# Kernel tuning notes

Hardware: AMD Instinct MI355X
Metric: run time of the kernel (lower is better)

The kernel has to match this reference:

```python
import jax, jax.numpy as jnp
import numpy as np

N, M, H, EMB, F = 2000, 32, 64, 32, 32   # nodes, neighbors, hidden, emb_dim, node_feat_dim
T, B, HOR = 12, 4, 12                     # seq_len, batch, horizon
K = 2                                     # tcn kernel
L_SAGE = 2
DILS = (1, 2)                             # dilations for the 2 TCN blocks


def _causal_conv(x, w, b, d):
    # x: (BN, C, T), w: (C_out, C_in, K) -- causal via left padding (K-1)*d
    y = jax.lax.conv_general_dilated(
        x, w, window_strides=(1,), padding=[((K - 1) * d, 0)],
        rhs_dilation=(d,), dimension_numbers=('NCH', 'OIH', 'NCH'))
    return y + b[None, :, None]


def setup_inputs() -> dict:
    key = jax.random.key(0)
    ks = jax.random.split(key, 32)
    s = 0.05
    def g(i, shape):
        return jax.random.normal(ks[i], shape, dtype=jnp.float32) * s
    return dict(
        inputs=jax.random.normal(ks[0], (T, B, N), dtype=jnp.float32),
        node_feas=jax.random.normal(ks[1], (N, F), dtype=jnp.float32),
        node_index=jax.random.randint(ks[2], (N, M), 0, N),
        # NodeEmbeddingMLP (fc3/fc4/fc5)
        w_fc3=g(3, (F, H)), b_fc3=jnp.zeros((H,), jnp.float32),
        w_fc4=g(4, (H, H)), b_fc4=jnp.zeros((H,), jnp.float32),
        w_fc5=g(5, (H, EMB)), b_fc5=jnp.zeros((EMB,), jnp.float32),
        # node_hidden_proj
        w_nhp=g(6, (EMB, H)), b_nhp=jnp.zeros((H,), jnp.float32),
        # attention (no bias)
        w_q=g(7, (EMB, H)), w_k=g(8, (EMB, H)),
        # input_proj
        w_in=g(9, (1, H)), b_in=jnp.zeros((H,), jnp.float32),
        # GraphSAGE layers (stacked)
        sage_w_self=g(10, (L_SAGE, H, H)), sage_b_self=jnp.zeros((L_SAGE, H), jnp.float32),
        sage_w_neigh=g(11, (L_SAGE, H, H)), sage_b_neigh=jnp.zeros((L_SAGE, H), jnp.float32),
        # TCN: 2 temporal blocks, each with conv1/conv2 (OIH layout)
        tcn_w1=g(12, (2, H, H, K)), tcn_b1=jnp.zeros((2, H), jnp.float32),
        tcn_w2=g(13, (2, H, H, K)), tcn_b2=jnp.zeros((2, H), jnp.float32),
        # scalar gate + output head
        w_gate=g(14, (H, 1)), b_gate=jnp.zeros((1,), jnp.float32),
        w_out=g(15, (H, HOR)), b_out=jnp.zeros((HOR,), jnp.float32),
    )


def reference(inputs, node_feas, node_index,
              w_fc3, b_fc3, w_fc4, b_fc4, w_fc5, b_fc5,
              w_nhp, b_nhp, w_q, w_k, w_in, b_in,
              sage_w_self, sage_b_self, sage_w_neigh, sage_b_neigh,
              tcn_w1, tcn_b1, tcn_w2, tcn_b2,
              w_gate, b_gate, w_out, b_out):
    # --- node embedding MLP ---
    e = jax.nn.relu(node_feas @ w_fc3 + b_fc3)
    e = jax.nn.relu(e @ w_fc4 + b_fc4)
    e = e @ w_fc5 + b_fc5                                  # (N, EMB)

    # --- attention over sampled neighbors (learned slim adjacency) ---
    q = e @ w_q                                            # (N, H)
    k = e[node_index] @ w_k                                # (N, M, H)
    scores = jnp.einsum('nh,nmh->nm', q, k) / jnp.sqrt(jnp.float32(H))
    w_adj = jax.nn.softmax(scores, axis=1)                 # (N, M) rows sum to 1

    node_hidden = e @ w_nhp + b_nhp                        # (N, H)

    # --- reshape inputs: (T, B, N) -> (B, T, N, 1) ---
    x = jnp.transpose(inputs, (1, 0, 2)).reshape(B, T, N, 1)
    x_proj = x @ w_in + b_in                               # (B, T, N, H)
    fused = x_proj + node_hidden                           # broadcast (N, H)
    h = fused.reshape(B * T, N, H)

    # --- GraphSAGE encoder: gather neighbors, weighted aggregate ---
    for l in range(L_SAGE):
        nb = h[:, node_index]                              # (B*T, N, M, H) irregular gather
        agg = jnp.einsum('nm,bnmh->bnh', w_adj, nb)        # (B*T, N, H)
        h = jax.nn.relu(h @ sage_w_self[l] + sage_b_self[l]
                        + agg @ sage_w_neigh[l] + sage_b_neigh[l])

    mid_output = h.reshape(B, T, N, H)

    # --- TCN over time per node: (B*N, H, T) ---
    ht = jnp.transpose(mid_output, (0, 2, 3, 1)).reshape(B * N, H, T)
    for l in range(2):
        res = ht
        y = jax.nn.relu(_causal_conv(ht, tcn_w1[l], tcn_b1[l], DILS[l]))
        y = jax.nn.relu(_causal_conv(y, tcn_w2[l], tcn_b2[l], DILS[l]))
        ht = jax.nn.relu(y + res)

    h_t = ht[:, :, -1]                                     # (B*N, H) last step temporal
    h_s = mid_output[:, -1].reshape(B * N, H)              # (B*N, H) last step spatial
    gate = jax.nn.sigmoid(h_t @ w_gate + b_gate)           # (B*N, 1) scalar gate
    fused_out = gate * h_t + (1.0 - gate) * h_s

    out = fused_out @ w_out + b_out                        # (B*N, HOR)
    outputs = out.reshape(B, N, HOR).transpose(2, 0, 1).reshape(HOR, B, N)
    return outputs, mid_output, w_adj
```

## Files before the change

### kernel.cpp

```cpp
#include <hip/hip_runtime.h>
#include <math.h>


__global__ __launch_bounds__(256) void k_embed(
    const float* __restrict__ nf, const float* __restrict__ inputs,
    const float* __restrict__ w3, const float* __restrict__ b3,
    const float* __restrict__ w4, const float* __restrict__ b4,
    const float* __restrict__ w5, const float* __restrict__ b5,
    const float* __restrict__ wq, const float* __restrict__ wk,
    const float* __restrict__ wn, const float* __restrict__ bn,
    const float* __restrict__ b_in,
    const float* __restrict__ tw1, const float* __restrict__ tw2,
    const float* __restrict__ sws, const float* __restrict__ swn,
    float4* __restrict__ wt4, float4* __restrict__ wsg,
    float* __restrict__ qo, float* __restrict__ eko, float* __restrict__ nho,
    float* __restrict__ xT)
{
    const int tid = threadIdx.x;
    if (tid < 192) {
        const int id = blockIdx.x * 192 + tid;
        const int t = id / 8000, rem = id % 8000;
        const int b = rem / 2000, n2 = rem % 2000;
        xT[n2 * 48 + b * 12 + t] = inputs[id];
    }
    if (blockIdx.x < 32) {
        const int id = blockIdx.x * 256 + tid;
        const int c = id >> 11, rr = id & 2047;
        const int p = rr >> 6, o = rr & 63;
        const float* src = (c == 0) ? tw1 : (c == 1) ? tw2
                         : (c == 2) ? tw1 + 8192 : tw2 + 8192;
        wt4[id] = *(const float4*)(src + o * 128 + p * 4);
    } else if (blockIdx.x < 48) {
        const int id = (blockIdx.x - 32) * 256 + tid;
        const int l = id >> 11, rr = id & 2047;
        const int k2 = rr >> 6, h = rr & 63;
        const float* S = sws + l * 4096;
        const float* Nn = swn + l * 4096;
        wsg[id] = make_float4(S[(2 * k2) * 64 + h],     Nn[(2 * k2) * 64 + h],
                              S[(2 * k2 + 1) * 64 + h], Nn[(2 * k2 + 1) * 64 + h]);
    }
    const int lane = tid & 63;
    const int n = blockIdx.x * 4 + (tid >> 6);

    float nfv = 0.f;
    if (lane < 32) nfv = nf[n * 32 + lane];

    float e1 = b3[lane];
#pragma unroll
    for (int f = 0; f < 32; ++f)
        e1 = fmaf(__shfl(nfv, f), w3[f * 64 + lane], e1);
    e1 = fmaxf(e1, 0.f);

    float e2 = b4[lane];
#pragma unroll
    for (int f = 0; f < 64; ++f)
        e2 = fmaf(__shfl(e1, f), w4[f * 64 + lane], e2);
    e2 = fmaxf(e2, 0.f);

    const int c = lane & 31;
    float ev = b5[c];
#pragma unroll
    for (int f = 0; f < 64; ++f)
        ev = fmaf(__shfl(e2, f), w5[f * 32 + c], ev);

    float qv = 0.f, ekv = 0.f, nhv = bn[lane] + b_in[lane];
#pragma unroll
    for (int f = 0; f < 32; ++f) {
        float e = __shfl(ev, f);
        qv  = fmaf(e, wq[f * 64 + lane], qv);
        ekv = fmaf(e, wk[f * 64 + lane], ekv);
        nhv = fmaf(e, wn[f * 64 + lane], nhv);
    }
    qo [n * 64 + lane] = qv;
    eko[n * 64 + lane] = ekv;
    nho[n * 64 + lane] = nhv;
}

__global__ __launch_bounds__(256) void k_front(
    const float* __restrict__ q, const float* __restrict__ ek,
    const float* __restrict__ xT, const float* __restrict__ nh2,
    const int* __restrict__ nidx,
    const float* __restrict__ sws, const float* __restrict__ sbs,
    const float* __restrict__ swn, const float* __restrict__ sbn,
    const float* __restrict__ w_in, const float4* __restrict__ wsg,
    float* __restrict__ wadj, float2* __restrict__ xa,
    float* __restrict__ base1, float* __restrict__ vecs)
{
    const int tid = threadIdx.x;
    const int lane = tid & 63, wave = tid >> 6;
    if (blockIdx.x == 500) {
        if (wave == 0) {
            const float wv = w_in[lane];
            float s1 = 0.f, n1 = 0.f;
#pragma unroll
            for (int k = 0; k < 64; ++k) {
                const float wkk = __shfl(wv, k);
                s1 = fmaf(wkk, sws[k * 64 + lane], s1);
                n1 = fmaf(wkk, swn[k * 64 + lane], n1);
            }
            vecs[lane] = s1; vecs[64 + lane] = n1;
        }
        return;
    }
    __shared__ __align__(16) float2 pair[4][64];
    const int n = blockIdx.x * 4 + wave;

    int j = 0;
    if (lane < 32) j = nidx[n * 32 + lane];
    float w;
    {
        const float4* qr = (const float4*)(q + n * 64);
        const float4* er = (const float4*)(ek + j * 64);
        float s = 0.f;
#pragma unroll
        for (int u = 0; u < 16; ++u) {
            const float4 a = qr[u], b = er[u];
            s = fmaf(a.x, b.x, s); s = fmaf(a.y, b.y, s);
            s = fmaf(a.z, b.z, s); s = fmaf(a.w, b.w, s);
        }
        s *= 0.125f;
        float mx = s;
#pragma unroll
        for (int d = 16; d >= 1; d >>= 1) mx = fmaxf(mx, __shfl_xor(mx, d));
        const float ex = expf(s - mx);
        float sum = ex;
#pragma unroll
        for (int d = 16; d >= 1; d >>= 1) sum += __shfl_xor(sum, d);
        w = ex / sum;
        if (lane < 32) wadj[n * 32 + lane] = w;
    }
    float ax = 0.f, anh = 0.f;
    const bool act = lane < 48;
#pragma unroll 8
    for (int m = 0; m < 32; ++m) {
        const int jm = __shfl(j, m);
        const float wm = __shfl(w, m);
        const float xv = act ? xT[jm * 48 + lane] : 0.f;
        ax  = fmaf(wm, xv, ax);
        anh = fmaf(wm, nh2[jm * 64 + lane], anh);
    }
    if (act) xa[n * 48 + lane] = make_float2(xT[n * 48 + lane], ax);
    pair[wave][lane] = make_float2(nh2[n * 64 + lane], anh);
    __syncthreads();

    float acc = sbs[lane] + sbn[lane];
    const float2* pw = pair[wave];
#pragma unroll
    for (int k2 = 0; k2 < 32; ++k2) {
        const float4 wv = wsg[k2 * 64 + lane];
        const float4 sv = *(const float4*)(pw + k2 * 2);
        acc = fmaf(sv.x, wv.x, acc); acc = fmaf(sv.y, wv.y, acc);
        acc = fmaf(sv.z, wv.z, acc); acc = fmaf(sv.w, wv.w, acc);
    }
    base1[n * 64 + lane] = acc;
}

__global__ __launch_bounds__(512, 8) void k_sage2(
    const float* __restrict__ base1, const float2* __restrict__ xa,
    const float* __restrict__ vecs,
    const int* __restrict__ nidx, const float* __restrict__ wadj,
    const float4* __restrict__ wsg2,
    const float* __restrict__ sbs, const float* __restrict__ sbn,
    float* __restrict__ mid)
{
    __shared__ __align__(16) float2 svp[48][64];
    const int tid = threadIdx.x, lane = tid & 63;
    const int wave = __builtin_amdgcn_readfirstlane(tid >> 6);
    const int n = blockIdx.x;
    const int bt0 = wave * 6;

    const float s1 = vecs[lane], n1 = vecs[64 + lane];
    const float bs = base1[n * 64 + lane];

    float agg[6] = {0.f, 0.f, 0.f, 0.f, 0.f, 0.f};
#pragma unroll 8
    for (int m = 0; m < 32; ++m) {
        const int j = nidx[n * 32 + m];
        const float w = wadj[n * 32 + m];
        const float bj = base1[j * 64 + lane];
        const float4* xr = (const float4*)(xa + j * 48 + bt0);
        const float4 p0 = xr[0], p1 = xr[1], p2 = xr[2];
        float t;
        t = fmaf(p0.x, s1, fmaf(p0.y, n1, bj)); agg[0] = fmaf(w, fmaxf(t, 0.f), agg[0]);
        t = fmaf(p0.z, s1, fmaf(p0.w, n1, bj)); agg[1] = fmaf(w, fmaxf(t, 0.f), agg[1]);
        t = fmaf(p1.x, s1, fmaf(p1.y, n1, bj)); agg[2] = fmaf(w, fmaxf(t, 0.f), agg[2]);
        t = fmaf(p1.z, s1, fmaf(p1.w, n1, bj)); agg[3] = fmaf(w, fmaxf(t, 0.f), agg[3]);
        t = fmaf(p2.x, s1, fmaf(p2.y, n1, bj)); agg[4] = fmaf(w, fmaxf(t, 0.f), agg[4]);
        t = fmaf(p2.z, s1, fmaf(p2.w, n1, bj)); agg[5] = fmaf(w, fmaxf(t, 0.f), agg[5]);
    }
    {
        const float4* xs = (const float4*)(xa + n * 48 + bt0);
        const float4 q0 = xs[0], q1 = xs[1], q2 = xs[2];
        svp[bt0 + 0][lane] = make_float2(fmaxf(fmaf(q0.x, s1, fmaf(q0.y, n1, bs)), 0.f), agg[0]);
        svp[bt0 + 1][lane] = make_float2(fmaxf(fmaf(q0.z, s1, fmaf(q0.w, n1, bs)), 0.f), agg[1]);
        svp[bt0 + 2][lane] = make_float2(fmaxf(fmaf(q1.x, s1, fmaf(q1.y, n1, bs)), 0.f), agg[2]);
        svp[bt0 + 3][lane] = make_float2(fmaxf(fmaf(q1.z, s1, fmaf(q1.w, n1, bs)), 0.f), agg[3]);
        svp[bt0 + 4][lane] = make_float2(fmaxf(fmaf(q2.x, s1, fmaf(q2.y, n1, bs)), 0.f), agg[4]);
        svp[bt0 + 5][lane] = make_float2(fmaxf(fmaf(q2.z, s1, fmaf(q2.w, n1, bs)), 0.f), agg[5]);
    }
    const float b2 = sbs[64 + lane] + sbn[64 + lane];
    float acc[6] = {b2, b2, b2, b2, b2, b2};
    const float4* wp = wsg2 + lane;
    const float2* s0 = svp[bt0];
#pragma unroll
    for (int k2 = 0; k2 < 32; ++k2) {
        const float4 w4 = wp[k2 * 64];
        const float4 v0 = *(const float4*)(s0 + 0 * 64 + k2 * 2);
        const float4 v1 = *(const float4*)(s0 + 1 * 64 + k2 * 2);
        const float4 v2 = *(const float4*)(s0 + 2 * 64 + k2 * 2);
        const float4 v3 = *(const float4*)(s0 + 3 * 64 + k2 * 2);
        const float4 v4 = *(const float4*)(s0 + 4 * 64 + k2 * 2);
        const float4 v5 = *(const float4*)(s0 + 5 * 64 + k2 * 2);
        acc[0] = fmaf(v0.x, w4.x, fmaf(v0.y, w4.y, fmaf(v0.z, w4.z, fmaf(v0.w, w4.w, acc[0]))));
        acc[1] = fmaf(v1.x, w4.x, fmaf(v1.y, w4.y, fmaf(v1.z, w4.z, fmaf(v1.w, w4.w, acc[1]))));
        acc[2] = fmaf(v2.x, w4.x, fmaf(v2.y, w4.y, fmaf(v2.z, w4.z, fmaf(v2.w, w4.w, acc[2]))));
        acc[3] = fmaf(v3.x, w4.x, fmaf(v3.y, w4.y, fmaf(v3.z, w4.z, fmaf(v3.w, w4.w, acc[3]))));
        acc[4] = fmaf(v4.x, w4.x, fmaf(v4.y, w4.y, fmaf(v4.z, w4.z, fmaf(v4.w, w4.w, acc[4]))));
        acc[5] = fmaf(v5.x, w4.x, fmaf(v5.y, w4.y, fmaf(v5.z, w4.z, fmaf(v5.w, w4.w, acc[5]))));
    }
#pragma unroll
    for (int r = 0; r < 6; ++r)
        mid[((bt0 + r) * 2000 + n) * 64 + lane] = fmaxf(acc[r], 0.f);
}

__global__ __launch_bounds__(256, 8) void k_tcn(
    const float* __restrict__ mid, const float4* __restrict__ wt4,
    const float* __restrict__ tb1, const float* __restrict__ tb2,
    const float* __restrict__ wgate, const float* __restrict__ bgate,
    const float* __restrict__ wout, const float* __restrict__ bout,
    float* __restrict__ outp)
{
    __shared__ __align__(16) float buf[4][7][68];
    const int tid = threadIdx.x, lane = tid & 63;
    const int wv = __builtin_amdgcn_readfirstlane(tid >> 6);
    const int seq = blockIdx.x * 4 + wv;
    const int b = seq / 2000, n = seq - b * 2000;
    const float* __restrict__ xb = mid + ((long)(b * 12) * 2000 + n) * 64;

    const float r0 = xb[ 7 * 128000 + lane];
    const float r1 = xb[ 9 * 128000 + lane];
    const float r2 = xb[11 * 128000 + lane];

    const float bs1 = tb1[lane];
    float y1[6] = {bs1, bs1, bs1, bs1, bs1, bs1};
    const float* __restrict__ xs = xb + 5 * 128000;
#pragma unroll 4
    for (int ig = 0; ig < 16; ++ig) {
        const float4 wA = wt4[(ig * 2 + 0) * 64 + lane];
        const float4 wB = wt4[(ig * 2 + 1) * 64 + lane];
        float4 xu[7];
#pragma unroll
        for (int u = 0; u < 7; ++u)
            xu[u] = *(const float4*)(xs + u * 128000 + ig * 4);
#pragma unroll
        for (int j = 0; j < 6; ++j) {
            float acc = y1[j];
            acc = fmaf(wA.x, xu[j].x, acc); acc = fmaf(wA.y, xu[j + 1].x, acc);
            acc = fmaf(wA.z, xu[j].y, acc); acc = fmaf(wA.w, xu[j + 1].y, acc);
            acc = fmaf(wB.x, xu[j].z, acc); acc = fmaf(wB.y, xu[j + 1].z, acc);
            acc = fmaf(wB.z, xu[j].w, acc); acc = fmaf(wB.w, xu[j + 1].w, acc);
            y1[j] = acc;
        }
    }
#pragma unroll
    for (int j = 0; j < 6; ++j)
        buf[wv][j][lane] = fmaxf(y1[j], 0.f);

    const float bs2 = tb2[lane];
    float a0 = bs2, a1 = bs2, a2 = bs2;
#pragma unroll 4
    for (int ig = 0; ig < 16; ++ig) {
        const float4 wA = wt4[2048 + (ig * 2 + 0) * 64 + lane];
        const float4 wB = wt4[2048 + (ig * 2 + 1) * 64 + lane];
        float4 yv[6];
#pragma unroll
        for (int j = 0; j < 6; ++j)
            yv[j] = *(const float4*)&buf[wv][j][ig * 4];
        a0 = fmaf(wA.x, yv[0].x, a0); a0 = fmaf(wA.y, yv[1].x, a0);
        a0 = fmaf(wA.z, yv[0].y, a0); a0 = fmaf(wA.w, yv[1].y, a0);
        a0 = fmaf(wB.x, yv[0].z, a0); a0 = fmaf(wB.y, yv[1].z, a0);
        a0 = fmaf(wB.z, yv[0].w, a0); a0 = fmaf(wB.w, yv[1].w, a0);
        a1 = fmaf(wA.x, yv[2].x, a1); a1 = fmaf(wA.y, yv[3].x, a1);
        a1 = fmaf(wA.z, yv[2].y, a1); a1 = fmaf(wA.w, yv[3].y, a1);
        a1 = fmaf(wB.x, yv[2].z, a1); a1 = fmaf(wB.y, yv[3].z, a1);
        a1 = fmaf(wB.z, yv[2].w, a1); a1 = fmaf(wB.w, yv[3].w, a1);
        a2 = fmaf(wA.x, yv[4].x, a2); a2 = fmaf(wA.y, yv[5].x, a2);
        a2 = fmaf(wA.z, yv[4].y, a2); a2 = fmaf(wA.w, yv[5].y, a2);
        a2 = fmaf(wB.x, yv[4].z, a2); a2 = fmaf(wB.y, yv[5].z, a2);
        a2 = fmaf(wB.z, yv[4].w, a2); a2 = fmaf(wB.w, yv[5].w, a2);
    }
    const float x20 = fmaxf(fmaxf(a0, 0.f) + r0, 0.f);
    const float x21 = fmaxf(fmaxf(a1, 0.f) + r1, 0.f);
    const float x22 = fmaxf(fmaxf(a2, 0.f) + r2, 0.f);
    buf[wv][0][lane] = x20;
    buf[wv][1][lane] = x21;
    buf[wv][2][lane] = x22;

    const float bs3 = tb1[64 + lane];
    float d0 = bs3, d1 = bs3;
#pragma unroll 4
    for (int ig = 0; ig < 16; ++ig) {
        const float4 wA = wt4[4096 + (ig * 2 + 0) * 64 + lane];
        const float4 wB = wt4[4096 + (ig * 2 + 1) * 64 + lane];
        const float4 x0 = *(const float4*)&buf[wv][0][ig * 4];
        const float4 x1 = *(const float4*)&buf[wv][1][ig * 4];
        const float4 x2 = *(const float4*)&buf[wv][2][ig * 4];
        d0 = fmaf(wA.x, x0.x, d0); d0 = fmaf(wA.y, x1.x, d0);
        d0 = fmaf(wA.z, x0.y, d0); d0 = fmaf(wA.w, x1.y, d0);
        d0 = fmaf(wB.x, x0.z, d0); d0 = fmaf(wB.y, x1.z, d0);
        d0 = fmaf(wB.z, x0.w, d0); d0 = fmaf(wB.w, x1.w, d0);
        d1 = fmaf(wA.x, x1.x, d1); d1 = fmaf(wA.y, x2.x, d1);
        d1 = fmaf(wA.z, x1.y, d1); d1 = fmaf(wA.w, x2.y, d1);
        d1 = fmaf(wB.x, x1.z, d1); d1 = fmaf(wB.y, x2.z, d1);
        d1 = fmaf(wB.z, x1.w, d1); d1 = fmaf(wB.w, x2.w, d1);
    }
    buf[wv][4][lane] = fmaxf(d0, 0.f);
    buf[wv][5][lane] = fmaxf(d1, 0.f);

    const float bs4 = tb2[64 + lane];
    float f = bs4;
#pragma unroll 4
    for (int ig = 0; ig < 16; ++ig) {
        const float4 wA = wt4[6144 + (ig * 2 + 0) * 64 + lane];
        const float4 wB = wt4[6144 + (ig * 2 + 1) * 64 + lane];
        const float4 g0 = *(const float4*)&buf[wv][4][ig * 4];
        const float4 g1 = *(const float4*)&buf[wv][5][ig * 4];
        f = fmaf(wA.x, g0.x, f); f = fmaf(wA.y, g1.x, f);
        f = fmaf(wA.z, g0.y, f); f = fmaf(wA.w, g1.y, f);
        f = fmaf(wB.x, g0.z, f); f = fmaf(wB.y, g1.z, f);
        f = fmaf(wB.z, g0.w, f); f = fmaf(wB.w, g1.w, f);
    }

    const float ht = fmaxf(fmaxf(f, 0.f) + x22, 0.f);
    float p = ht * wgate[lane];
#pragma unroll
    for (int dd = 1; dd < 64; dd <<= 1) p += __shfl_xor(p, dd);
    const float g = 1.f / (1.f + expf(-(p + bgate[0])));
    buf[wv][6][lane] = g * ht + (1.f - g) * r2;
    if (lane < 12) {
        float acc = bout[lane];
#pragma unroll 4
        for (int ig = 0; ig < 16; ++ig) {
            const float4 f4 = *(const float4*)&buf[wv][6][ig * 4];
            acc = fmaf(f4.x, wout[(ig * 4 + 0) * 12 + lane], acc);
            acc = fmaf(f4.y, wout[(ig * 4 + 1) * 12 + lane], acc);
            acc = fmaf(f4.z, wout[(ig * 4 + 2) * 12 + lane], acc);
            acc = fmaf(f4.w, wout[(ig * 4 + 3) * 12 + lane], acc);
        }
        outp[lane * 8000 + seq] = acc;
    }
}

extern "C" void kernel_launch(void* const* d_in, const int* in_sizes, int n_in,
                              void* d_out, int out_size, void* d_ws, size_t ws_size,
                              hipStream_t stream) {
    const float* inputs     = (const float*)d_in[0];
    const float* node_feas  = (const float*)d_in[1];
    const int*   node_index = (const int*)  d_in[2];
    const float* w_fc3 = (const float*)d_in[3];
    const float* b_fc3 = (const float*)d_in[4];
    const float* w_fc4 = (const float*)d_in[5];
    const float* b_fc4 = (const float*)d_in[6];
    const float* w_fc5 = (const float*)d_in[7];
    const float* b_fc5 = (const float*)d_in[8];
    const float* w_nhp = (const float*)d_in[9];
    const float* b_nhp = (const float*)d_in[10];
    const float* w_q   = (const float*)d_in[11];
    const float* w_k   = (const float*)d_in[12];
    const float* w_in  = (const float*)d_in[13];
    const float* b_in  = (const float*)d_in[14];
    const float* sws   = (const float*)d_in[15];
    const float* sbs   = (const float*)d_in[16];
    const float* swn   = (const float*)d_in[17];
    const float* sbn   = (const float*)d_in[18];
    const float* tw1   = (const float*)d_in[19];
    const float* tb1   = (const float*)d_in[20];
    const float* tw2   = (const float*)d_in[21];
    const float* tb2   = (const float*)d_in[22];
    const float* wgate = (const float*)d_in[23];
    const float* bgate = (const float*)d_in[24];
    const float* wout  = (const float*)d_in[25];
    const float* bout  = (const float*)d_in[26];

    float* out  = (float*)d_out;
    float* mid  = out + 96000;
    float* wadj = mid + 6144000;

    float*  q     = (float*)d_ws;
    float*  ek    = q     + 128000;
    float*  nh2   = ek    + 128000;
    float*  base1 = nh2   + 128000;
    float*  xT    = base1 + 128000;
    float2* xa    = (float2*)(xT + 96000);
    float*  vecs  = xT + 96000 + 192000;
    float4* wt4   = (float4*)(vecs + 128);
    float4* wsg   = (float4*)(vecs + 128 + 32768);

    k_embed<<<500, 256, 0, stream>>>(node_feas, inputs, w_fc3, b_fc3, w_fc4, b_fc4,
                                     w_fc5, b_fc5, w_q, w_k, w_nhp, b_nhp, b_in,
                                     tw1, tw2, sws, swn, wt4, wsg,
                                     q, ek, nh2, xT);
    k_front<<<501, 256, 0, stream>>>(q, ek, xT, nh2, node_index,
                                     sws, sbs, swn, sbn, w_in, wsg,
                                     wadj, xa, base1, vecs);
    k_sage2<<<2000, 512, 0, stream>>>(base1, xa, vecs, node_index, wadj,
                                      wsg + 2048, sbs, sbn, mid);
    k_tcn<<<2000, 256, 0, stream>>>(mid, wt4, tb1, tb2,
                                    wgate, bgate, wout, bout, out);
}
```

Baseline: 125.1 us.

## Fuse TCN stage into SAGE layer-2 kernel using shared-memory node tile

Merges the separate TCN kernel into k_sage2. Each block keeps its node's 48 time-batch rows of mid in shared memory, and two waves then run the four causal convolutions, the gate and the output head from LDS instead of rereading mid from global memory. The TCN weights are repacked into a float2 layout so each lane computes two output channels for one batch, and the head reduction becomes a cross-lane shuffle over 12 outputs. This removes a kernel launch and the global reread of mid. The cost is that six of the eight waves idle during the TCN phase, and the larger shared-memory footprint may lower occupancy.

After: 137.7 us. 1.1x slower.

```diff
diff --git a/kernel.cpp b/kernel.cpp
--- a/kernel.cpp
+++ b/kernel.cpp
@@ -12,7 +12,7 @@
     const float* __restrict__ b_in,
     const float* __restrict__ tw1, const float* __restrict__ tw2,
     const float* __restrict__ sws, const float* __restrict__ swn,
-    float4* __restrict__ wt4, float4* __restrict__ wsg,
+    float2* __restrict__ W2, float4* __restrict__ wsg,
     float* __restrict__ qo, float* __restrict__ eko, float* __restrict__ nho,
     float* __restrict__ xT)
 {
@@ -23,15 +23,16 @@
         const int b = rem / 2000, n2 = rem % 2000;
         xT[n2 * 48 + b * 12 + t] = inputs[id];
     }
-    if (blockIdx.x < 32) {
+    if (blockIdx.x < 64) {
         const int id = blockIdx.x * 256 + tid;
-        const int c = id >> 11, rr = id & 2047;
-        const int p = rr >> 6, o = rr & 63;
+        const int c = id >> 12, r = id & 4095;
+        const int ig = r >> 8, o = (r >> 2) & 63, ii = r & 3;
         const float* src = (c == 0) ? tw1 : (c == 1) ? tw2
                          : (c == 2) ? tw1 + 8192 : tw2 + 8192;
-        wt4[id] = *(const float4*)(src + o * 128 + p * 4);
-    } else if (blockIdx.x < 48) {
-        const int id = (blockIdx.x - 32) * 256 + tid;
+        const int i = ig * 4 + ii;
+        W2[id] = make_float2(src[o * 128 + i * 2], src[o * 128 + i * 2 + 1]);
+    } else if (blockIdx.x < 80) {
+        const int id = (blockIdx.x - 64) * 256 + tid;
         const int l = id >> 11, rr = id & 2047;
         const int k2 = rr >> 6, h = rr & 63;
         const float* S = sws + l * 4096;
@@ -155,199 +156,249 @@
     base1[n * 64 + lane] = acc;
 }
 
+__device__ __forceinline__ float conv8(float acc, const float4 wA, const float4 wB,
+                                       const float4 xl, const float4 xr)
+{
+    acc = fmaf(wA.x, xl.x, acc); acc = fmaf(wA.y, xr.x, acc);
+    acc = fmaf(wA.z, xl.y, acc); acc = fmaf(wA.w, xr.y, acc);
+    acc = fmaf(wB.x, xl.z, acc); acc = fmaf(wB.y, xr.z, acc);
+    acc = fmaf(wB.z, xl.w, acc); acc = fmaf(wB.w, xr.w, acc);
+    return acc;
+}
+
 __global__ __launch_bounds__(512, 8) void k_sage2(
     const float* __restrict__ base1, const float2* __restrict__ xa,
     const float* __restrict__ vecs,
     const int* __restrict__ nidx, const float* __restrict__ wadj,
     const float4* __restrict__ wsg2,
     const float* __restrict__ sbs, const float* __restrict__ sbn,
-    float* __restrict__ mid)
-{
-    __shared__ __align__(16) float2 svp[48][64];
-    const int tid = threadIdx.x, lane = tid & 63;
-    const int wave = __builtin_amdgcn_readfirstlane(tid >> 6);
-    const int n = blockIdx.x;
-    const int bt0 = wave * 6;
-
-    const float s1 = vecs[lane], n1 = vecs[64 + lane];
-    const float bs = base1[n * 64 + lane];
-
-    float agg[6] = {0.f, 0.f, 0.f, 0.f, 0.f, 0.f};
-#pragma unroll 8
-    for (int m = 0; m < 32; ++m) {
-        const int j = nidx[n * 32 + m];
-        const float w = wadj[n * 32 + m];
-        const float bj = base1[j * 64 + lane];
-        const float4* xr = (const float4*)(xa + j * 48 + bt0);
-        const float4 p0 = xr[0], p1 = xr[1], p2 = xr[2];
-        float t;
-        t = fmaf(p0.x, s1, fmaf(p0.y, n1, bj)); agg[0] = fmaf(w, fmaxf(t, 0.f), agg[0]);
-        t = fmaf(p0.z, s1, fmaf(p0.w, n1, bj)); agg[1] = fmaf(w, fmaxf(t, 0.f), agg[1]);
-        t = fmaf(p1.x, s1, fmaf(p1.y, n1, bj)); agg[2] = fmaf(w, fmaxf(t, 0.f), agg[2]);
-        t = fmaf(p1.z, s1, fmaf(p1.w, n1, bj)); agg[3] = fmaf(w, fmaxf(t, 0.f), agg[3]);
-        t = fmaf(p2.x, s1, fmaf(p2.y, n1, bj)); agg[4] = fmaf(w, fmaxf(t, 0.f), agg[4]);
-        t = fmaf(p2.z, s1, fmaf(p2.w, n1, bj)); agg[5] = fmaf(w, fmaxf(t, 0.f), agg[5]);
-    }
-    {
-        const float4* xs = (const float4*)(xa + n * 48 + bt0);
-        const float4 q0 = xs[0], q1 = xs[1], q2 = xs[2];
-        svp[bt0 + 0][lane] = make_float2(fmaxf(fmaf(q0.x, s1, fmaf(q0.y, n1, bs)), 0.f), agg[0]);
-        svp[bt0 + 1][lane] = make_float2(fmaxf(fmaf(q0.z, s1, fmaf(q0.w, n1, bs)), 0.f), agg[1]);
-        svp[bt0 + 2][lane] = make_float2(fmaxf(fmaf(q1.x, s1, fmaf(q1.y, n1, bs)), 0.f), agg[2]);
-        svp[bt0 + 3][lane] = make_float2(fmaxf(fmaf(q1.z, s1, fmaf(q1.w, n1, bs)), 0.f), agg[3]);
-        svp[bt0 + 4][lane] = make_float2(fmaxf(fmaf(q2.x, s1, fmaf(q2.y, n1, bs)), 0.f), agg[4]);
-        svp[bt0 + 5][lane] = make_float2(fmaxf(fmaf(q2.z, s1, fmaf(q2.w, n1, bs)), 0.f), agg[5]);
-    }
-    const float b2 = sbs[64 + lane] + sbn[64 + lane];
-    float acc[6] = {b2, b2, b2, b2, b2, b2};
-    const float4* wp = wsg2 + lane;
-    const float2* s0 = svp[bt0];
-#pragma unroll
-    for (int k2 = 0; k2 < 32; ++k2) {
-        const float4 w4 = wp[k2 * 64];
-        const float4 v0 = *(const float4*)(s0 + 0 * 64 + k2 * 2);
-        const float4 v1 = *(const float4*)(s0 + 1 * 64 + k2 * 2);
-        const float4 v2 = *(const float4*)(s0 + 2 * 64 + k2 * 2);
-        const float4 v3 = *(const float4*)(s0 + 3 * 64 + k2 * 2);
-        const float4 v4 = *(const float4*)(s0 + 4 * 64 + k2 * 2);
-        const float4 v5 = *(const float4*)(s0 + 5 * 64 + k2 * 2);
-        acc[0] = fmaf(v0.x, w4.x, fmaf(v0.y, w4.y, fmaf(v0.z, w4.z, fmaf(v0.w, w4.w, acc[0]))));
-        acc[1] = fmaf(v1.x, w4.x, fmaf(v1.y, w4.y, fmaf(v1.z, w4.z, fmaf(v1.w, w4.w, acc[1]))));
-        acc[2] = fmaf(v2.x, w4.x, fmaf(v2.y, w4.y, fmaf(v2.z, w4.z, fmaf(v2.w, w4.w, acc[2]))));
-        acc[3] = fmaf(v3.x, w4.x, fmaf(v3.y, w4.y, fmaf(v3.z, w4.z, fmaf(v3.w, w4.w, acc[3]))));
-        acc[4] = fmaf(v4.x, w4.x, fmaf(v4.y, w4.y, fmaf(v4.z, w4.z, fmaf(v4.w, w4.w, acc[4]))));
-        acc[5] = fmaf(v5.x, w4.x, fmaf(v5.y, w4.y, fmaf(v5.z, w4.z, fmaf(v5.w, w4.w, acc[5]))));
-    }
-#pragma unroll
-    for (int r = 0; r < 6; ++r)
-        mid[((bt0 + r) * 2000 + n) * 64 + lane] = fmaxf(acc[r], 0.f);
-}
-
-__global__ __launch_bounds__(256, 8) void k_tcn(
-    const float* __restrict__ mid, const float4* __restrict__ wt4,
+    const float2* __restrict__ W2,
     const float* __restrict__ tb1, const float* __restrict__ tb2,
     const float* __restrict__ wgate, const float* __restrict__ bgate,
     const float* __restrict__ wout, const float* __restrict__ bout,
-    float* __restrict__ outp)
+    float* __restrict__ mid, float* __restrict__ outp)
 {
-    __shared__ __align__(16) float buf[4][7][68];
+    __shared__ __align__(16) float pool[6144 + 3264];
+    float2* svp  = (float2*)pool;
+    float*  xls2 = pool + 6144;
+    float*  scr  = pool;
+
     const int tid = threadIdx.x, lane = tid & 63;
-    const int wv = __builtin_amdgcn_readfirstlane(tid >> 6);
-    const int seq = blockIdx.x * 4 + wv;
-    const int b = seq / 2000, n = seq - b * 2000;
-    const float* __restrict__ xb = mid + ((long)(b * 12) * 2000 + n) * 64;
-
-    const float r0 = xb[ 7 * 128000 + lane];
-    const float r1 = xb[ 9 * 128000 + lane];
-    const float r2 = xb[11 * 128000 + lane];
-
-    const float bs1 = tb1[lane];
-    float y1[6] = {bs1, bs1, bs1, bs1, bs1, bs1};
-    const float* __restrict__ xs = xb + 5 * 128000;
+    const int wfl = __builtin_amdgcn_readfirstlane(tid >> 6);
+    const int n = blockIdx.x;
+    const int bt0 = wfl * 6;
+
+    {
+        const float s1 = vecs[lane], n1 = vecs[64 + lane];
+        const float bs = base1[n * 64 + lane];
+
+        float agg[6] = {0.f, 0.f, 0.f, 0.f, 0.f, 0.f};
+#pragma unroll 8
+        for (int m = 0; m < 32; ++m) {
+            const int j = nidx[n * 32 + m];
+            const float w = wadj[n * 32 + m];
+            const float bj = base1[j * 64 + lane];
+            const float4* xr = (const float4*)(xa + j * 48 + bt0);
+            const float4 p0 = xr[0], p1 = xr[1], p2 = xr[2];
+            float t;
+            t = fmaf(p0.x, s1, fmaf(p0.y, n1, bj)); agg[0] = fmaf(w, fmaxf(t, 0.f), agg[0]);
+            t = fmaf(p0.z, s1, fmaf(p0.w, n1, bj)); agg[1] = fmaf(w, fmaxf(t, 0.f), agg[1]);
+            t = fmaf(p1.x, s1, fmaf(p1.y, n1, bj)); agg[2] = fmaf(w, fmaxf(t, 0.f), agg[2]);
+            t = fmaf(p1.z, s1, fmaf(p1.w, n1, bj)); agg[3] = fmaf(w, fmaxf(t, 0.f), agg[3]);
+            t = fmaf(p2.x, s1, fmaf(p2.y, n1, bj)); agg[4] = fmaf(w, fmaxf(t, 0.f), agg[4]);
+            t = fmaf(p2.z, s1, fmaf(p2.w, n1, bj)); agg[5] = fmaf(w, fmaxf(t, 0.f), agg[5]);
+        }
+        {
+            const float4* xs = (const float4*)(xa + n * 48 + bt0);
+            const float4 q0 = xs[0], q1 = xs[1], q2 = xs[2];
+            svp[(bt0 + 0) * 64 + lane] = make_float2(fmaxf(fmaf(q0.x, s1, fmaf(q0.y, n1, bs)), 0.f), agg[0]);
+            svp[(bt0 + 1) * 64 + lane] = make_float2(fmaxf(fmaf(q0.z, s1, fmaf(q0.w, n1, bs)), 0.f), agg[1]);
+            svp[(bt0 + 2) * 64 + lane] = make_float2(fmaxf(fmaf(q1.x, s1, fmaf(q1.y, n1, bs)), 0.f), agg[2]);
+            svp[(bt0 + 3) * 64 + lane] = make_float2(fmaxf(fmaf(q1.z, s1, fmaf(q1.w, n1, bs)), 0.f), agg[3]);
+            svp[(bt0 + 4) * 64 + lane] = make_float2(fmaxf(fmaf(q2.x, s1, fmaf(q2.y, n1, bs)), 0.f), agg[4]);
+            svp[(bt0 + 5) * 64 + lane] = make_float2(fmaxf(fmaf(q2.z, s1, fmaf(q2.w, n1, bs)), 0.f), agg[5]);
+        }
+        const float b2 = sbs[64 + lane] + sbn[64 + lane];
+        float acc[6] = {b2, b2, b2, b2, b2, b2};
+        const float4* wp = wsg2 + lane;
+        const float2* s0 = svp + bt0 * 64;
+#pragma unroll
+        for (int k2 = 0; k2 < 32; ++k2) {
+            const float4 w4 = wp[k2 * 64];
+            const float4 v0 = *(const float4*)(s0 + 0 * 64 + k2 * 2);
+            const float4 v1 = *(const float4*)(s0 + 1 * 64 + k2 * 2);
+            const float4 v2 = *(const float4*)(s0 + 2 * 64 + k2 * 2);
+            const float4 v3 = *(const float4*)(s0 + 3 * 64 + k2 * 2);
+            const float4 v4 = *(const float4*)(s0 + 4 * 64 + k2 * 2);
+            const float4 v5 = *(const float4*)(s0 + 5 * 64 + k2 * 2);
+            acc[0] = fmaf(v0.x, w4.x, fmaf(v0.y, w4.y, fmaf(v0.z, w4.z, fmaf(v0.w, w4.w, acc[0]))));
+            acc[1] = fmaf(v1.x, w4.x, fmaf(v1.y, w4.y, fmaf(v1.z, w4.z, fmaf(v1.w, w4.w, acc[1]))));
+            acc[2] = fmaf(v2.x, w4.x, fmaf(v2.y, w4.y, fmaf(v2.z, w4.z, fmaf(v2.w, w4.w, acc[2]))));
+            acc[3] = fmaf(v3.x, w4.x, fmaf(v3.y, w4.y, fmaf(v3.z, w4.z, fmaf(v3.w, w4.w, acc[3]))));
+            acc[4] = fmaf(v4.x, w4.x, fmaf(v4.y, w4.y, fmaf(v4.z, w4.z, fmaf(v4.w, w4.w, acc[4]))));
+            acc[5] = fmaf(v5.x, w4.x, fmaf(v5.y, w4.y, fmaf(v5.z, w4.z, fmaf(v5.w, w4.w, acc[5]))));
+        }
+#pragma unroll
+        for (int r = 0; r < 6; ++r) {
+            const float mv = fmaxf(acc[r], 0.f);
+            mid[((bt0 + r) * 2000 + n) * 64 + lane] = mv;
+            xls2[(bt0 + r) * 68 + lane] = mv;
+        }
+    }
+    __syncthreads();
+    if (wfl >= 2) return;
+
+    const int h = lane >> 1;
+    const int sl = lane & 1;
+    const int b = wfl * 2 + sl;
+    const int obase = h * 2;
+    const float* __restrict__ xrow = xls2 + b * 12 * 68;
+    const float4* __restrict__ Wf4 = (const float4*)W2;
+
+    float y[2][6];
+    {
+        const float2 bv = *(const float2*)(tb1 + obase);
+#pragma unroll
+        for (int j = 0; j < 6; ++j) { y[0][j] = bv.x; y[1][j] = bv.y; }
+    }
 #pragma unroll 4
     for (int ig = 0; ig < 16; ++ig) {
-        const float4 wA = wt4[(ig * 2 + 0) * 64 + lane];
-        const float4 wB = wt4[(ig * 2 + 1) * 64 + lane];
-        float4 xu[7];
-#pragma unroll
-        for (int u = 0; u < 7; ++u)
-            xu[u] = *(const float4*)(xs + u * 128000 + ig * 4);
-#pragma unroll
-        for (int j = 0; j < 6; ++j) {
-            float acc = y1[j];
-            acc = fmaf(wA.x, xu[j].x, acc); acc = fmaf(wA.y, xu[j + 1].x, acc);
-            acc = fmaf(wA.z, xu[j].y, acc); acc = fmaf(wA.w, xu[j + 1].y, acc);
-            acc = fmaf(wB.x, xu[j].z, acc); acc = fmaf(wB.y, xu[j + 1].z, acc);
-            acc = fmaf(wB.z, xu[j].w, acc); acc = fmaf(wB.w, xu[j + 1].w, acc);
-            y1[j] = acc;
-        }
-    }
-#pragma unroll
-    for (int j = 0; j < 6; ++j)
-        buf[wv][j][lane] = fmaxf(y1[j], 0.f);
-
-    const float bs2 = tb2[lane];
-    float a0 = bs2, a1 = bs2, a2 = bs2;
+        const float4 wA0 = Wf4[(ig * 64 + obase + 0) * 2 + 0];
+        const float4 wB0 = Wf4[(ig * 64 + obase + 0) * 2 + 1];
+        const float4 wA1 = Wf4[(ig * 64 + obase + 1) * 2 + 0];
+        const float4 wB1 = Wf4[(ig * 64 + obase + 1) * 2 + 1];
+        {
+            const float4 x5 = *(const float4*)(xrow +  5 * 68 + ig * 4);
+            const float4 x6 = *(const float4*)(xrow +  6 * 68 + ig * 4);
+            const float4 x7 = *(const float4*)(xrow +  7 * 68 + ig * 4);
+            const float4 x8 = *(const float4*)(xrow +  8 * 68 + ig * 4);
+            y[0][0] = conv8(y[0][0], wA0, wB0, x5, x6); y[1][0] = conv8(y[1][0], wA1, wB1, x5, x6);
+            y[0][1] = conv8(y[0][1], wA0, wB0, x6, x7); y[1][1] = conv8(y[1][1], wA1, wB1, x6, x7);
+            y[0][2] = conv8(y[0][2], wA0, wB0, x7, x8); y[1][2] = conv8(y[1][2], wA1, wB1, x7, x8);
+        }
+        {
+            const float4 x8 = *(const float4*)(xrow +  8 * 68 + ig * 4);
+            const float4 x9 = *(const float4*)(xrow +  9 * 68 + ig * 4);
+            const float4 xa2 = *(const float4*)(xrow + 10 * 68 + ig * 4);
+            const float4 xb2 = *(const float4*)(xrow + 11 * 68 + ig * 4);
+            y[0][3] = conv8(y[0][3], wA0, wB0, x8, x9);  y[1][3] = conv8(y[1][3], wA1, wB1, x8, x9);
+            y[0][4] = conv8(y[0][4], wA0, wB0, x9, xa2); y[1][4] = conv8(y[1][4], wA1, wB1, x9, xa2);
+            y[0][5] = conv8(y[0][5], wA0, wB0, xa2, xb2); y[1][5] = conv8(y[1][5], wA1, wB1, xa2, xb2);
+        }
+    }
+#pragma unroll
+    for (int j = 0; j < 6; ++j) {
+        float2 o2;
+        o2.x = fmaxf(y[0][j], 0.f); o2.y = fmaxf(y[1][j], 0.f);
+        *(float2*)&scr[(j * 4 + b) * 68 + obase] = o2;
+    }
+
+    float a2[2][3];
+    {
+        const float2 bv = *(const float2*)(tb2 + obase);
+#pragma unroll
+        for (int v = 0; v < 3; ++v) { a2[0][v] = bv.x; a2[1][v] = bv.y; }
+    }
 #pragma unroll 4
     for (int ig = 0; ig < 16; ++ig) {
-        const float4 wA = wt4[2048 + (ig * 2 + 0) * 64 + lane];
-        const float4 wB = wt4[2048 + (ig * 2 + 1) * 64 + lane];
-        float4 yv[6];
-#pragma unroll
-        for (int j = 0; j < 6; ++j)
-            yv[j] = *(const float4*)&buf[wv][j][ig * 4];
-        a0 = fmaf(wA.x, yv[0].x, a0); a0 = fmaf(wA.y, yv[1].x, a0);
-        a0 = fmaf(wA.z, yv[0].y, a0); a0 = fmaf(wA.w, yv[1].y, a0);
-        a0 = fmaf(wB.x, yv[0].z, a0); a0 = fmaf(wB.y, yv[1].z, a0);
-        a0 = fmaf(wB.z, yv[0].w, a0); a0 = fmaf(wB.w, yv[1].w, a0);
-        a1 = fmaf(wA.x, yv[2].x, a1); a1 = fmaf(wA.y, yv[3].x, a1);
-        a1 = fmaf(wA.z, yv[2].y, a1); a1 = fmaf(wA.w, yv[3].y, a1);
-        a1 = fmaf(wB.x, yv[2].z, a1); a1 = fmaf(wB.y, yv[3].z, a1);
-        a1 = fmaf(wB.z, yv[2].w, a1); a1 = fmaf(wB.w, yv[3].w, a1);
-        a2 = fmaf(wA.x, yv[4].x, a2); a2 = fmaf(wA.y, yv[5].x, a2);
-        a2 = fmaf(wA.z, yv[4].y, a2); a2 = fmaf(wA.w, yv[5].y, a2);
-        a2 = fmaf(wB.x, yv[4].z, a2); a2 = fmaf(wB.y, yv[5].z, a2);
-        a2 = fmaf(wB.z, yv[4].w, a2); a2 = fmaf(wB.w, yv[5].w, a2);
-    }
-    const float x20 = fmaxf(fmaxf(a0, 0.f) + r0, 0.f);
-    const float x21 = fmaxf(fmaxf(a1, 0.f) + r1, 0.f);
-    const float x22 = fmaxf(fmaxf(a2, 0.f) + r2, 0.f);
-    buf[wv][0][lane] = x20;
-    buf[wv][1][lane] = x21;
-    buf[wv][2][lane] = x22;
-
-    const float bs3 = tb1[64 + lane];
-    float d0 = bs3, d1 = bs3;
+        const float4 wA0 = Wf4[((16 + ig) * 64 + obase + 0) * 2 + 0];
+        const float4 wB0 = Wf4[((16 + ig) * 64 + obase + 0) * 2 + 1];
+        const float4 wA1 = Wf4[((16 + ig) * 64 + obase + 1) * 2 + 0];
+        const float4 wB1 = Wf4[((16 + ig) * 64 + obase + 1) * 2 + 1];
+#pragma unroll
+        for (int v = 0; v < 3; ++v) {
+            const float4 pl = *(const float4*)&scr[((2 * v) * 4 + b) * 68 + ig * 4];
+            const float4 pr = *(const float4*)&scr[((2 * v + 1) * 4 + b) * 68 + ig * 4];
+            a2[0][v] = conv8(a2[0][v], wA0, wB0, pl, pr);
+            a2[1][v] = conv8(a2[1][v], wA1, wB1, pl, pr);
+        }
+    }
+    float x22_0, x22_1;
+    {
+        const int TT[3] = {7, 9, 11};
+#pragma unroll
+        for (int v = 0; v < 3; ++v) {
+            const float2 xr2 = *(const float2*)(xrow + TT[v] * 68 + obase);
+            float2 o2;
+            o2.x = fmaxf(fmaxf(a2[0][v], 0.f) + xr2.x, 0.f);
+            o2.y = fmaxf(fmaxf(a2[1][v], 0.f) + xr2.y, 0.f);
+            *(float2*)&scr[((6 + v) * 4 + b) * 68 + obase] = o2;
+            if (v == 2) { x22_0 = o2.x; x22_1 = o2.y; }
+        }
+    }
+
+    float d3[2][2];
+    {
+        const float2 bv = *(const float2*)(tb1 + 64 + obase);
+        d3[0][0] = bv.x; d3[0][1] = bv.x; d3[1][0] = bv.y; d3[1][1] = bv.y;
+    }
 #pragma unroll 4
     for (int ig = 0; ig < 16; ++ig) {
-        const float4 wA = wt4[4096 + (ig * 2 + 0) * 64 + lane];
-        const float4 wB = wt4[4096 + (ig * 2 + 1) * 64 + lane];
-        const float4 x0 = *(const float4*)&buf[wv][0][ig * 4];
-        const float4 x1 = *(const float4*)&buf[wv][1][ig * 4];
-        const float4 x2 = *(const float4*)&buf[wv][2][ig * 4];
-        d0 = fmaf(wA.x, x0.x, d0); d0 = fmaf(wA.y, x1.x, d0);
-        d0 = fmaf(wA.z, x0.y, d0); d0 = fmaf(wA.w, x1.y, d0);
-        d0 = fmaf(wB.x, x0.z, d0); d0 = fmaf(wB.y, x1.z, d0);
-        d0 = fmaf(wB.z, x0.w, d0); d0 = fmaf(wB.w, x1.w, d0);
-        d1 = fmaf(wA.x, x1.x, d1); d1 = fmaf(wA.y, x2.x, d1);
-        d1 = fmaf(wA.z, x1.y, d1); d1 = fmaf(wA.w, x2.y, d1);
-        d1 = fmaf(wB.x, x1.z, d1); d1 = fmaf(wB.y, x2.z, d1);
-        d1 = fmaf(wB.z, x1.w, d1); d1 = fmaf(wB.w, x2.w, d1);
-    }
-    buf[wv][4][lane] = fmaxf(d0, 0.f);
-    buf[wv][5][lane] = fmaxf(d1, 0.f);
-
-    const float bs4 = tb2[64 + lane];
-    float f = bs4;
+        const float4 wA0 = Wf4[((32 + ig) * 64 + obase + 0) * 2 + 0];
+        const float4 wB0 = Wf4[((32 + ig) * 64 + obase + 0) * 2 + 1];
+        const float4 wA1 = Wf4[((32 + ig) * 64 + obase + 1) * 2 + 0];
+        const float4 wB1 = Wf4[((32 + ig) * 64 + obase + 1) * 2 + 1];
+        const float4 p0 = *(const float4*)&scr[(6 * 4 + b) * 68 + ig * 4];
+        const float4 p1 = *(const float4*)&scr[(7 * 4 + b) * 68 + ig * 4];
+        const float4 p2 = *(const float4*)&scr[(8 * 4 + b) * 68 + ig * 4];
+        d3[0][0] = conv8(d3[0][0], wA0, wB0, p0, p1);
+        d3[1][0] = conv8(d3[1][0], wA1, wB1, p0, p1);
+        d3[0][1] = conv8(d3[0][1], wA0, wB0, p1, p2);
+        d3[1][1] = conv8(d3[1][1], wA1, wB1, p1, p2);
+    }
+    {
+        float2 o2;
+        o2.x = fmaxf(d3[0][0], 0.f); o2.y = fmaxf(d3[1][0], 0.f);
+        *(float2*)&scr[(9 * 4 + b) * 68 + obase] = o2;
+        o2.x = fmaxf(d3[0][1], 0.f); o2.y = fmaxf(d3[1][1], 0.f);
+        *(float2*)&scr[(10 * 4 + b) * 68 + obase] = o2;
+    }
+
+    float f0, f1;
+    {
+        const float2 bv = *(const float2*)(tb2 + 64 + obase);
+        f0 = bv.x; f1 = bv.y;
+    }
 #pragma unroll 4
     for (int ig = 0; ig < 16; ++ig) {
-        const float4 wA = wt4[6144 + (ig * 2 + 0) * 64 + lane];
-        const float4 wB = wt4[6144 + (ig * 2 + 1) * 64 + lane];
-        const float4 g0 = *(const float4*)&buf[wv][4][ig * 4];
-        const float4 g1 = *(const float4*)&buf[wv][5][ig * 4];
-        f = fmaf(wA.x, g0.x, f); f = fmaf(wA.y, g1.x, f);
-        f = fmaf(wA.z, g0.y, f); f = fmaf(wA.w, g1.y, f);
-        f = fmaf(wB.x, g0.z, f); f = fmaf(wB.y, g1.z, f);
-        f = fmaf(wB.z, g0.w, f); f = fmaf(wB.w, g1.w, f);
-    }
-
-    const float ht = fmaxf(fmaxf(f, 0.f) + x22, 0.f);
-    float p = ht * wgate[lane];
-#pragma unroll
-    for (int dd = 1; dd < 64; dd <<= 1) p += __shfl_xor(p, dd);
+        const float4 wA0 = Wf4[((48 + ig) * 64 + obase + 0) * 2 + 0];
+        const float4 wB0 = Wf4[((48 + ig) * 64 + obase + 0) * 2 + 1];
+        const float4 wA1 = Wf4[((48 + ig) * 64 + obase + 1) * 2 + 0];
+        const float4 wB1 = Wf4[((48 + ig) * 64 + obase + 1) * 2 + 1];
+        const float4 g0 = *(const float4*)&scr[(9 * 4 + b) * 68 + ig * 4];
+        const float4 g1 = *(const float4*)&scr[(10 * 4 + b) * 68 + ig * 4];
+        f0 = conv8(f0, wA0, wB0, g0, g1);
+        f1 = conv8(f1, wA1, wB1, g0, g1);
+    }
+    const float ht0 = fmaxf(fmaxf(f0, 0.f) + x22_0, 0.f);
+    const float ht1 = fmaxf(fmaxf(f1, 0.f) + x22_1, 0.f);
+
+    const float2 wg2 = *(const float2*)(wgate + obase);
+    float p = ht0 * wg2.x + ht1 * wg2.y;
+#pragma unroll
+    for (int d = 2; d < 64; d <<= 1) p += __shfl_xor(p, d);
     const float g = 1.f / (1.f + expf(-(p + bgate[0])));
-    buf[wv][6][lane] = g * ht + (1.f - g) * r2;
-    if (lane < 12) {
-        float acc = bout[lane];
-#pragma unroll 4
-        for (int ig = 0; ig < 16; ++ig) {
-            const float4 f4 = *(const float4*)&buf[wv][6][ig * 4];
-            acc = fmaf(f4.x, wout[(ig * 4 + 0) * 12 + lane], acc);
-            acc = fmaf(f4.y, wout[(ig * 4 + 1) * 12 + lane], acc);
-            acc = fmaf(f4.z, wout[(ig * 4 + 2) * 12 + lane], acc);
-            acc = fmaf(f4.w, wout[(ig * 4 + 3) * 12 + lane], acc);
-        }
-        outp[lane * 8000 + seq] = acc;
+    const float2 hs = *(const float2*)(xrow + 11 * 68 + obase);
+    const float fo0 = g * ht0 + (1.f - g) * hs.x;
+    const float fo1 = g * ht1 + (1.f - g) * hs.y;
+
+    float po[12];
+    {
+        const float* wr0 = wout + (obase + 0) * 12;
+        const float* wr1 = wout + (obase + 1) * 12;
+#pragma unroll
+        for (int h2 = 0; h2 < 12; ++h2)
+            po[h2] = fo0 * wr0[h2] + fo1 * wr1[h2];
+    }
+#pragma unroll
+    for (int d = 2; d < 64; d <<= 1) {
+#pragma unroll
+        for (int h2 = 0; h2 < 12; ++h2) po[h2] += __shfl_xor(po[h2], d);
+    }
+    if (h == 0) {
+#pragma unroll
+        for (int h2 = 0; h2 < 12; ++h2)
+            outp[h2 * 8000 + b * 2000 + n] = po[h2] + bout[h2];
     }
 }
 
@@ -393,18 +444,18 @@
     float*  xT    = base1 + 128000;
     float2* xa    = (float2*)(xT + 96000);
     float*  vecs  = xT + 96000 + 192000;
-    float4* wt4   = (float4*)(vecs + 128);
+    float2* W2    = (float2*)(vecs + 128);
     float4* wsg   = (float4*)(vecs + 128 + 32768);
 
     k_embed<<<500, 256, 0, stream>>>(node_feas, inputs, w_fc3, b_fc3, w_fc4, b_fc4,
                                      w_fc5, b_fc5, w_q, w_k, w_nhp, b_nhp, b_in,
-                                     tw1, tw2, sws, swn, wt4, wsg,
+                                     tw1, tw2, sws, swn, W2, wsg,
                                      q, ek, nh2, xT);
     k_front<<<501, 256, 0, stream>>>(q, ek, xT, nh2, node_index,
                                      sws, sbs, swn, sbn, w_in, wsg,
                                      wadj, xa, base1, vecs);
     k_sage2<<<2000, 512, 0, stream>>>(base1, xa, vecs, node_index, wadj,
-                                      wsg + 2048, sbs, sbn, mid);
-    k_tcn<<<2000, 256, 0, stream>>>(mid, wt4, tb1, tb2,
-                                    wgate, bgate, wout, bout, out);
+                                      wsg + 2048, sbs, sbn,
+                                      W2, tb1, tb2, wgate, bgate, wout, bout,
+                                      mid, out);
 }
```
